# Kernel optimization log

Hardware: AMD Instinct MI355X
Metric: run time of the kernel (lower is better)

The kernel has to match this reference:

```python
import jax, jax.numpy as jnp
import numpy as np

C = 2048
EPS = 1e-12


def conv1x1(x, w, b):
    # x: [B,C_in,H,W], w: [C_out,C_in], b: [C_out]
    return jnp.einsum('oc,bchw->bohw', w, x) + b[None, :, None, None]


def unfold3x3(x):
    # torch F.unfold(kernel=3, padding=1): output [B, C*9, H*W],
    # feature order (c, ki, kj) with c slowest.
    B, Cc, H, W = x.shape
    xp = jnp.pad(x, ((0, 0), (0, 0), (1, 1), (1, 1)))
    patches = jnp.stack([xp[:, :, ki:ki + H, kj:kj + W]
                         for ki in range(3) for kj in range(3)], axis=2)  # [B,C,9,H,W]
    return patches.reshape(B, Cc * 9, H * W)


def fold3x3(u, H, W):
    # torch F.fold(kernel=3, padding=1): overlap-add. u: [B, C*9, H*W]
    B = u.shape[0]
    Cc = u.shape[1] // 9
    t = u.reshape(B, Cc, 3, 3, H, W)
    out = jnp.zeros((B, Cc, H + 2, W + 2), dtype=u.dtype)
    for ki in range(3):
        for kj in range(3):
            out = out.at[:, :, ki:ki + H, kj:kj + W].add(t[:, :, ki, kj])
    return out[:, :, 1:1 + H, 1:1 + W]


def l2norm(x, axis):
    n = jnp.sqrt(jnp.sum(x * x, axis=axis, keepdims=True))
    return x / jnp.maximum(n, EPS)


def setup_inputs() -> dict:
    key = jax.random.key(0)
    ks = jax.random.split(key, 8)
    B, H, W = 4, 24, 24
    s = 0.02
    return {
        'part_ref': jax.random.normal(ks[0], (B, C, H, W), jnp.float32),
        'part_target': jax.random.normal(ks[1], (B, C, H, W), jnp.float32),
        'wq': jax.random.normal(ks[2], (C, C), jnp.float32) * s,
        'bq': jnp.zeros((C,), jnp.float32),
        'wk': jax.random.normal(ks[3], (C, C), jnp.float32) * s,
        'bk': jnp.zeros((C,), jnp.float32),
        'wt': jax.random.normal(ks[4], (C, 2 * C), jnp.float32) * s,
        'bt': jnp.zeros((C,), jnp.float32),
    }


def reference(part_ref, part_target, wq, bq, wk, bk, wt, bt):
    B, _, H, W = part_ref.shape
    part_target_o = part_target
    k = conv1x1(part_ref, wk, bk)
    q = conv1x1(part_target, wq, bq)

    tgt_unf = unfold3x3(q)        # [B, C*9, L]
    ref_unf1 = unfold3x3(k)       # [B, C*9, L]

    ref_n = l2norm(jnp.transpose(ref_unf1, (0, 2, 1)), axis=2)  # [B, L, C*9]
    tgt_n = l2norm(tgt_unf, axis=1)                              # [B, C*9, L]

    R = jnp.einsum('blc,bcm->blm', ref_n, tgt_n)  # [B, L_ref, L_tgt]
    R_star = jnp.max(R, axis=1)                   # [B, L]
    R_arg = jnp.argmax(R, axis=1)                 # [B, L]

    # gather best ref patch per target location along dim 2
    T_unf = jnp.take_along_axis(ref_unf1, R_arg[:, None, :], axis=2)  # [B, C*9, L]
    T_part = fold3x3(T_unf, H, W) / 9.0

    S = R_star.reshape(B, 1, H, W)
    x_res = jnp.concatenate((q, T_part), axis=1)  # [B, 2C, H, W]
    res = conv1x1(x_res, wt, bt) * S + part_target_o
    return res
```

## Files before the change

kernel.cpp:

```cpp
#include <hip/hip_runtime.h>
#include <cstddef>
#include <cstdint>

#define LPIX 576
#define CCH  2048
#define NB   4

typedef __attribute__((ext_vector_type(8))) short short8;
typedef __attribute__((ext_vector_type(4))) float f32x4;
typedef __attribute__((ext_vector_type(4))) unsigned short u16x4;

__device__ __forceinline__ unsigned short f2bf(float f) {
    uint32_t u = __builtin_bit_cast(uint32_t, f);
    u += 0x7fff + ((u >> 16) & 1);
    return (unsigned short)(u >> 16);
}
__device__ __forceinline__ float bf2f(unsigned short s) {
    return __builtin_bit_cast(float, (uint32_t)s << 16);
}

__device__ __forceinline__ void gload_lds16(const void* g, void* l) {
    __builtin_amdgcn_global_load_lds((const __attribute__((address_space(1))) void*)g,
                                     (__attribute__((address_space(3))) void*)l, 16, 0, 0);
}

template<int BM, int BN>
__device__ __forceinline__ void mm_core64(
    const short* __restrict__ Ab, int lda,
    const short* __restrict__ Bb, int ldb,
    int k0, int kend, short* As, short* Bs,
    int m0, int n0, f32x4 (&acc)[BM/32][BN/32])
{
    const int tid  = threadIdx.x;
    const int lane = tid & 63;
    const int w    = tid >> 6;
    const int wm = (w & 1) * (BM / 2);
    const int wn = (w >> 1) * (BN / 2);
    const int l15 = lane & 15;
    const int k8  = (lane >> 4) * 8;
    const int r   = tid >> 2;
    const int kk  = (tid & 3) * 8;

    const short* Aptr[BM / 32]; short* Alds[BM / 32];
    #pragma unroll
    for (int u = 0; u < BM / 32; ++u) {
        const int p = u & 1, g = u >> 1;
        Aptr[u] = Ab + (size_t)(m0 + g * 64 + r) * lda + p * 32 + kk;
        Alds[u] = As + p * BM * 32 + g * 2048 + tid * 8;
    }
    const short* Bptr[BN / 32]; short* Blds[BN / 32];
    #pragma unroll
    for (int u = 0; u < BN / 32; ++u) {
        const int p = u & 1, g = u >> 1;
        Bptr[u] = Bb + (size_t)(n0 + g * 64 + r) * ldb + p * 32 + kk;
        Blds[u] = Bs + p * BN * 32 + g * 2048 + tid * 8;
    }

    for (int c0 = k0; c0 < kend; c0 += 64) {
        #pragma unroll
        for (int u = 0; u < BM / 32; ++u) gload_lds16(Aptr[u] + c0, Alds[u]);
        #pragma unroll
        for (int u = 0; u < BN / 32; ++u) gload_lds16(Bptr[u] + c0, Blds[u]);
        __syncthreads();
        #pragma unroll
        for (int s = 0; s < 2; ++s) {
            short8 fa[BM / 32], fb[BN / 32];
            #pragma unroll
            for (int i = 0; i < BM / 32; ++i)
                fa[i] = *(const short8*)(As + s * BM * 32 + (wm + i * 16 + l15) * 32 + k8);
            #pragma unroll
            for (int j = 0; j < BN / 32; ++j)
                fb[j] = *(const short8*)(Bs + s * BN * 32 + (wn + j * 16 + l15) * 32 + k8);
            #pragma unroll
            for (int i = 0; i < BM / 32; ++i)
                #pragma unroll
                for (int j = 0; j < BN / 32; ++j)
                    acc[i][j] = __builtin_amdgcn_mfma_f32_16x16x32_bf16(fa[i], fb[j], acc[i][j], 0, 0, 0);
        }
        __syncthreads();
    }
}

__global__ __launch_bounds__(256) void wcast2_k(const float* __restrict__ wq,
                                                const float* __restrict__ wk,
                                                short* __restrict__ Wb) {
    const float* W = blockIdx.y ? wk : wq;
    short* D = Wb + (size_t)blockIdx.y * CCH * CCH;
    int i = (blockIdx.x * 256 + threadIdx.x) * 4;
    float4 v = *(const float4*)(W + i);
    u16x4 u;
    u.x = f2bf(v.x); u.y = f2bf(v.y); u.z = f2bf(v.z); u.w = f2bf(v.w);
    *(u16x4*)(D + i) = u;
}

__global__ __launch_bounds__(256) void wcast_k(const float* __restrict__ W,
                                               short* __restrict__ Wb) {
    int i = (blockIdx.x * 256 + threadIdx.x) * 4;
    float4 v = *(const float4*)(W + i);
    u16x4 u;
    u.x = f2bf(v.x); u.y = f2bf(v.y); u.z = f2bf(v.z); u.w = f2bf(v.w);
    *(u16x4*)(Wb + i) = u;
}

__global__ __launch_bounds__(256) void tcast_k(const float* __restrict__ tgt,
                                               const float* __restrict__ ref,
                                               short* __restrict__ T1) {
    __shared__ float tile[32][33];
    const int z = blockIdx.z;
    const int b = z & 3, which = z >> 2;
    const float* X = (which ? ref : tgt) + (size_t)b * CCH * LPIX;
    const int c0 = blockIdx.y * 32;
    const int l0 = blockIdx.x * 32;
    const int tx = threadIdx.x, ty = threadIdx.y;
    #pragma unroll
    for (int j = 0; j < 4; ++j)
        tile[ty + j * 8][tx] = X[(size_t)(c0 + ty + j * 8) * LPIX + l0 + tx];
    __syncthreads();
    short* D = T1 + ((size_t)(which * NB + b) * LPIX) * CCH;
    #pragma unroll
    for (int j = 0; j < 4; ++j)
        D[(size_t)(l0 + ty + j * 8) * CCH + c0 + tx] = (short)f2bf(tile[tx][ty + j * 8]);
}

__global__ __launch_bounds__(256) void conv_k(
    const short* __restrict__ T1, const short* __restrict__ Wb,
    const float* __restrict__ bq, const float* __restrict__ bk,
    short* __restrict__ x2t, short* __restrict__ kt,
    float* __restrict__ nq, float* __restrict__ nk)
{
    __shared__ short As[64 * 64];
    __shared__ short Bs[128 * 64];
    const int id = blockIdx.x;
    const int xcd = id & 7, slot = id >> 3;
    const int sid = xcd * 4 + slot / 36;
    const int r36 = slot % 36;
    const int which = sid >> 4;
    const int m0 = (r36 % 9) * 64;
    const int n0 = (sid & 15) * 128;
    const int b  = r36 / 9;
    const short* Ab = T1 + (size_t)(which * NB + b) * LPIX * CCH;
    const short* Bb = Wb + (size_t)which * CCH * CCH;
    const float* bias = which ? bk : bq;
    short* Yb = which ? (kt + (size_t)b * LPIX * CCH) : (x2t + (size_t)b * LPIX * 4096);
    float* Nb = (which ? nk : nq) + b * LPIX;
    const int ldy = which ? CCH : 4096;
    f32x4 acc[2][4] = {};
    mm_core64<64, 128>(Ab, CCH, Bb, CCH, 0, CCH, As, Bs, m0, n0, acc);
    const int lane = threadIdx.x & 63, w = threadIdx.x >> 6;
    const int wm = (w & 1) * 32, wn = (w >> 1) * 64;
    const int l15 = lane & 15, quad = lane >> 4;
    float pv[2][4] = {};
    #pragma unroll
    for (int i = 0; i < 2; ++i)
        #pragma unroll
        for (int j = 0; j < 4; ++j) {
            const int gn = n0 + wn + j * 16 + l15;
            const float bi = bias[gn];
            #pragma unroll
            for (int r = 0; r < 4; ++r) {
                const int gm = m0 + wm + i * 16 + quad * 4 + r;
                float v = acc[i][j][r] + bi;
                pv[i][r] += v * v;
                Yb[(size_t)gm * ldy + gn] = (short)f2bf(v);
            }
        }
    #pragma unroll
    for (int i = 0; i < 2; ++i)
        #pragma unroll
        for (int r = 0; r < 4; ++r) {
            float s = pv[i][r];
            #pragma unroll
            for (int m = 1; m < 16; m <<= 1) s += __shfl_xor(s, m);
            if (l15 == 0) {
                const int gm = m0 + wm + i * 16 + quad * 4 + r;
                atomicAdd(&Nb[gm], s);
            }
        }
}

__global__ __launch_bounds__(256) void gram_k(
    const short* __restrict__ kt, const short* __restrict__ x2t,
    float* __restrict__ Mpart)
{
    __shared__ short As[64 * 64];
    __shared__ short Bs[64 * 64];
    const int z = blockIdx.z;
    const int b = z >> 1, kc = z & 1;
    const short* Ab = kt + (size_t)b * LPIX * CCH;
    const short* Bb = x2t + (size_t)b * LPIX * 4096;
    const int m0 = blockIdx.y * 64;
    const int n0 = blockIdx.x * 64;
    f32x4 acc[2][2] = {};
    mm_core64<64, 64>(Ab, CCH, Bb, 4096, kc * 1024, kc * 1024 + 1024, As, Bs, m0, n0, acc);
    float* Mb = Mpart + (size_t)(kc * NB + b) * LPIX * LPIX;
    const int lane = threadIdx.x & 63, w = threadIdx.x >> 6;
    const int wm = (w & 1) * 32, wn = (w >> 1) * 32;
    const int l15 = lane & 15, quad = lane >> 4;
    #pragma unroll
    for (int i = 0; i < 2; ++i)
        #pragma unroll
        for (int j = 0; j < 2; ++j) {
            const int gn = n0 + wn + j * 16 + l15;
            #pragma unroll
            for (int r = 0; r < 4; ++r) {
                const int gm = m0 + wm + i * 16 + quad * 4 + r;
                Mb[(size_t)gm * LPIX + gn] = acc[i][j][r];
            }
        }
}

__global__ __launch_bounds__(256) void fin_k(
    const short* __restrict__ wtb, const short* __restrict__ x2t,
    const float* __restrict__ bt, const float* __restrict__ S,
    const float* __restrict__ PT, float* __restrict__ out)
{
    __shared__ short As[128 * 64];
    __shared__ short Bs[64 * 64];
    const int id = blockIdx.x;
    const int xcd = id & 7, slot = id >> 3;
    const int hi = slot >= 36;
    const int r36 = slot - hi * 36;
    const int m0 = (xcd * 2 + hi) * 128;
    const int n0 = (r36 % 9) * 64;
    const int b  = r36 / 9;
    const short* Bb = x2t + (size_t)b * LPIX * 4096;
    f32x4 acc[4][2] = {};
    mm_core64<128, 64>(wtb, 4096, Bb, 4096, 0, 4096, As, Bs, m0, n0, acc);
    const int lane = threadIdx.x & 63, w = threadIdx.x >> 6;
    const int wm = (w & 1) * 64, wn = (w >> 1) * 32;
    const int l15 = lane & 15, quad = lane >> 4;
    #pragma unroll
    for (int i = 0; i < 4; ++i)
        #pragma unroll
        for (int j = 0; j < 2; ++j) {
            const int gn = n0 + wn + j * 16 + l15;
            const float sv = S[b * LPIX + gn];
            #pragma unroll
            for (int r = 0; r < 4; ++r) {
                const int gm = m0 + wm + i * 16 + quad * 4 + r;
                float v = (acc[i][j][r] + bt[gm]) * sv
                        + PT[((size_t)b * CCH + gm) * LPIX + gn];
                out[((size_t)b * CCH + gm) * LPIX + gn] = v;
            }
        }
}

__global__ __launch_bounds__(256) void argmax1_k(
    const float* __restrict__ Mpart, const float* __restrict__ nk,
    float* __restrict__ Pv, int* __restrict__ Pi)
{
    const int b   = blockIdx.z;
    const int lrb = blockIdx.y;
    const int tx = threadIdx.x, ty = threadIdx.y;
    const int tid = ty * 64 + tx;
    __shared__ float invNkS[24];
    if (tid < 24) {
        const int jr = tid;
        float s = 0.f;
        #pragma unroll
        for (int di = -1; di <= 1; ++di) {
            const int ii = lrb + di;
            if ((unsigned)ii > 23u) continue;
            #pragma unroll
            for (int dj = -1; dj <= 1; ++dj) {
                const int jj = jr + dj;
                if ((unsigned)jj > 23u) continue;
                s += nk[b * LPIX + ii * 24 + jj];
            }
        }
        invNkS[jr] = 1.0f / fmaxf(sqrtf(s), 1e-12f);
    }
    __syncthreads();
    const int lt = blockIdx.x * 64 + tx;
    const int it = lt / 24, jt = lt % 24;
    const float* Mb0 = Mpart + (size_t)b * LPIX * LPIX;
    const float* Mb1 = Mpart + (size_t)(NB + b) * LPIX * LPIX;
    float best = -1e30f; int bidx = 0;
    #pragma unroll
    for (int i = 0; i < 6; ++i) {
        const int jr = ty + i * 4;
        const int lr = lrb * 24 + jr;
        const int base = lr * LPIX + lt;
        float g = 0.f;
        #pragma unroll
        for (int di = -1; di <= 1; ++di) {
            if ((unsigned)(lrb + di) > 23u || (unsigned)(it + di) > 23u) continue;
            #pragma unroll
            for (int dj = -1; dj <= 1; ++dj) {
                if ((unsigned)(jr + dj) > 23u || (unsigned)(jt + dj) > 23u) continue;
                const int o = base + (di * 24 + dj) * (LPIX + 1);
                g += Mb0[o] + Mb1[o];
            }
        }
        float v = g * invNkS[jr];
        if (v > best) { best = v; bidx = lr; }
    }
    __shared__ float rv[4][64];
    __shared__ int   ri[4][64];
    rv[ty][tx] = best; ri[ty][tx] = bidx;
    __syncthreads();
    if (ty == 0) {
        #pragma unroll
        for (int y = 1; y < 4; ++y) {
            float v = rv[y][tx]; int id = ri[y][tx];
            if (v > best || (v == best && id < bidx)) { best = v; bidx = id; }
        }
        Pv[((size_t)b * 24 + lrb) * LPIX + lt] = best;
        Pi[((size_t)b * 24 + lrb) * LPIX + lt] = bidx;
    }
}

__global__ __launch_bounds__(256) void argmax2_k(
    const float* __restrict__ Pv, const int* __restrict__ Pi,
    const float* __restrict__ nq,
    float* __restrict__ S, int* __restrict__ Arg)
{
    int idx = blockIdx.x * 256 + threadIdx.x;
    if (idx >= NB * LPIX) return;
    int b = idx / LPIX, lt = idx % LPIX;
    int it = lt / 24, jt = lt % 24;
    float s = 0.f;
    #pragma unroll
    for (int di = -1; di <= 1; ++di) {
        const int ii = it + di;
        if ((unsigned)ii > 23u) continue;
        #pragma unroll
        for (int dj = -1; dj <= 1; ++dj) {
            const int jj = jt + dj;
            if ((unsigned)jj > 23u) continue;
            s += nq[b * LPIX + ii * 24 + jj];
        }
    }
    const float invNq = 1.0f / fmaxf(sqrtf(s), 1e-12f);
    float best = -1e30f; int bidx = 0;
    #pragma unroll
    for (int c = 0; c < 24; ++c) {
        float v = Pv[((size_t)b * 24 + c) * LPIX + lt];
        int  id = Pi[((size_t)b * 24 + c) * LPIX + lt];
        if (v > best || (v == best && id < bidx)) { best = v; bidx = id; }
    }
    S[idx]   = best * invNq;
    Arg[idx] = bidx;
}

__global__ __launch_bounds__(256) void gather_k(
    const short* __restrict__ kt, const int* __restrict__ Arg,
    short* __restrict__ x2t)
{
    const int id = blockIdx.x;
    const int xcd = id & 7, slot = id >> 3;
    const int b  = xcd >> 1;
    const int l0 = ((xcd & 1) * 72 + slot) * 4;
    const int lane = threadIdx.x, ty = threadIdx.y;
    const int tid = ty * 64 + lane;
    __shared__ int tap[4][9];
    if (tid < 36) {
        int px = tid / 9, t9 = tid % 9;
        int l = l0 + px;
        int i = l / 24, j = l % 24;
        int ki = t9 / 3, kj = t9 % 3;
        int ip = i + 1 - ki, jp = j + 1 - kj;
        int off = -1;
        if (ip >= 0 && ip < 24 && jp >= 0 && jp < 24) {
            int a = Arg[b * LPIX + ip * 24 + jp];
            int rr = a / 24 + ki - 1;
            int cc = a % 24 + kj - 1;
            if (rr >= 0 && rr < 24 && cc >= 0 && cc < 24) off = rr * 24 + cc;
        }
        tap[px][t9] = off;
    }
    __syncthreads();
    const int l = l0 + ty;
    const short* Kb = kt + (size_t)b * LPIX * CCH;
    short* dst = x2t + ((size_t)b * LPIX + l) * 4096 + CCH;
    int t[9];
    #pragma unroll
    for (int i = 0; i < 9; ++i) t[i] = tap[ty][i];
    const float inv9 = 1.0f / 9.0f;
    #pragma unroll
    for (int j = 0; j < 8; ++j) {
        int c = (lane + j * 64) * 4;
        float s0 = 0.f, s1 = 0.f, s2 = 0.f, s3 = 0.f;
        #pragma unroll
        for (int t9 = 0; t9 < 9; ++t9) {
            int off = t[t9];
            if (off < 0) continue;
            u16x4 u = *(const u16x4*)(Kb + (size_t)off * CCH + c);
            s0 += bf2f(u.x); s1 += bf2f(u.y); s2 += bf2f(u.z); s3 += bf2f(u.w);
        }
        u16x4 o;
        o.x = f2bf(s0 * inv9); o.y = f2bf(s1 * inv9);
        o.z = f2bf(s2 * inv9); o.w = f2bf(s3 * inv9);
        *(u16x4*)(dst + c) = o;
    }
}

extern "C" void kernel_launch(void* const* d_in, const int* in_sizes, int n_in,
                              void* d_out, int out_size, void* d_ws, size_t ws_size,
                              hipStream_t stream) {
    const float* part_ref = (const float*)d_in[0];
    const float* part_tgt = (const float*)d_in[1];
    const float* wq = (const float*)d_in[2];
    const float* bq = (const float*)d_in[3];
    const float* wk = (const float*)d_in[4];
    const float* bk = (const float*)d_in[5];
    const float* wt = (const float*)d_in[6];
    const float* bt = (const float*)d_in[7];
    float* out = (float*)d_out;

    short* wqb2 = (short*)d_ws;
    short* wtb  = wqb2;
    short* T1   = wqb2 + (size_t)2 * CCH * CCH;
    short* kt   = T1 + (size_t)2 * NB * LPIX * CCH;
    short* x2t  = kt + (size_t)NB * LPIX * CCH;
    float* Mpart = (float*)T1;
    float* nk    = (float*)(x2t + (size_t)NB * LPIX * 4096);
    float* nq    = nk + NB * LPIX;
    float* Sbuf  = nq + NB * LPIX;
    int*   Arg   = (int*)(Sbuf + NB * LPIX);
    float* Pv    = (float*)(Arg + NB * LPIX);
    int*   Pi    = (int*)(Pv + (size_t)24 * NB * LPIX);

    hipMemsetAsync(nk, 0, 2 * NB * LPIX * sizeof(float), stream);

    wcast2_k<<<dim3(4096, 2), 256, 0, stream>>>(wq, wk, wqb2);
    tcast_k<<<dim3(18, 64, 8), dim3(32, 8), 0, stream>>>(part_tgt, part_ref, T1);

    conv_k<<<1152, 256, 0, stream>>>(T1, wqb2, bq, bk, x2t, kt, nq, nk);

    gram_k<<<dim3(9, 9, 8), 256, 0, stream>>>(kt, x2t, Mpart);

    argmax1_k<<<dim3(9, 24, NB), dim3(64, 4), 0, stream>>>(Mpart, nk, Pv, Pi);
    argmax2_k<<<9, 256, 0, stream>>>(Pv, Pi, nq, Sbuf, Arg);

    gather_k<<<576, dim3(64, 4), 0, stream>>>(kt, Arg, x2t);

    wcast_k<<<8192, 256, 0, stream>>>(wt, wtb);
    fin_k<<<576, 256, 0, stream>>>(wtb, x2t, bt, Sbuf, part_tgt, out);
}
```

Measured before the change: 351.6 us.

## Merge batch into row dimension, use 128x128 tiles, split-K final conv with atomics

The conv kernel now treats all four batches as one 2304-row matrix and uses 128x128 tiles, halving the block count and raising reuse per loaded tile. The final 1x1 conv also uses 128x128 tiles over the merged pixel dimension, with K split in two and results accumulated into the output via float atomicAdd. A new init kernel first writes the bias*S + residual term to the output. This trades fewer, larger GEMM blocks for atomic traffic on the output, an extra full pass over it, and nondeterministic summation order.

```diff
diff --git a/kernel.cpp b/kernel.cpp
--- a/kernel.cpp
+++ b/kernel.cpp
@@ -5,6 +5,7 @@
 #define LPIX 576
 #define CCH  2048
 #define NB   4
+#define LROWS 2304
 
 typedef __attribute__((ext_vector_type(8))) short short8;
 typedef __attribute__((ext_vector_type(4))) float f32x4;
@@ -128,30 +129,27 @@
     short* __restrict__ x2t, short* __restrict__ kt,
     float* __restrict__ nq, float* __restrict__ nk)
 {
-    __shared__ short As[64 * 64];
+    __shared__ short As[128 * 64];
     __shared__ short Bs[128 * 64];
     const int id = blockIdx.x;
     const int xcd = id & 7, slot = id >> 3;
-    const int sid = xcd * 4 + slot / 36;
-    const int r36 = slot % 36;
+    const int sid = xcd * 4 + slot / 18;
+    const int r18 = slot % 18;
     const int which = sid >> 4;
-    const int m0 = (r36 % 9) * 64;
     const int n0 = (sid & 15) * 128;
-    const int b  = r36 / 9;
-    const short* Ab = T1 + (size_t)(which * NB + b) * LPIX * CCH;
+    const int m0 = r18 * 128;
+    const short* Ab = T1 + (size_t)which * LROWS * CCH;
     const short* Bb = Wb + (size_t)which * CCH * CCH;
     const float* bias = which ? bk : bq;
-    short* Yb = which ? (kt + (size_t)b * LPIX * CCH) : (x2t + (size_t)b * LPIX * 4096);
-    float* Nb = (which ? nk : nq) + b * LPIX;
-    const int ldy = which ? CCH : 4096;
-    f32x4 acc[2][4] = {};
-    mm_core64<64, 128>(Ab, CCH, Bb, CCH, 0, CCH, As, Bs, m0, n0, acc);
+    float* Nb = which ? nk : nq;
+    f32x4 acc[4][4] = {};
+    mm_core64<128, 128>(Ab, CCH, Bb, CCH, 0, CCH, As, Bs, m0, n0, acc);
     const int lane = threadIdx.x & 63, w = threadIdx.x >> 6;
-    const int wm = (w & 1) * 32, wn = (w >> 1) * 64;
+    const int wm = (w & 1) * 64, wn = (w >> 1) * 64;
     const int l15 = lane & 15, quad = lane >> 4;
-    float pv[2][4] = {};
-    #pragma unroll
-    for (int i = 0; i < 2; ++i)
+    float pv[4][4] = {};
+    #pragma unroll
+    for (int i = 0; i < 4; ++i)
         #pragma unroll
         for (int j = 0; j < 4; ++j) {
             const int gn = n0 + wn + j * 16 + l15;
@@ -161,11 +159,12 @@
                 const int gm = m0 + wm + i * 16 + quad * 4 + r;
                 float v = acc[i][j][r] + bi;
                 pv[i][r] += v * v;
-                Yb[(size_t)gm * ldy + gn] = (short)f2bf(v);
-            }
-        }
-    #pragma unroll
-    for (int i = 0; i < 2; ++i)
+                if (which) kt[(size_t)gm * CCH + gn] = (short)f2bf(v);
+                else       x2t[(size_t)gm * 4096 + gn] = (short)f2bf(v);
+            }
+        }
+    #pragma unroll
+    for (int i = 0; i < 4; ++i)
         #pragma unroll
         for (int r = 0; r < 4; ++r) {
             float s = pv[i][r];
@@ -209,38 +208,52 @@
         }
 }
 
+__global__ __launch_bounds__(256) void initout_k(
+    const float* __restrict__ bt, const float* __restrict__ S,
+    const float* __restrict__ PT, float* __restrict__ out)
+{
+    const int idx = blockIdx.x * 256 + threadIdx.x;
+    const int l4 = idx % 144;
+    const int o  = (idx / 144) % CCH;
+    const int b  = idx / (144 * CCH);
+    const float bi = bt[o];
+    float4 sv = *(const float4*)(S + b * LPIX + l4 * 4);
+    float4 pv = *(const float4*)(PT + ((size_t)b * CCH + o) * LPIX + l4 * 4);
+    float4 ov;
+    ov.x = bi * sv.x + pv.x; ov.y = bi * sv.y + pv.y;
+    ov.z = bi * sv.z + pv.z; ov.w = bi * sv.w + pv.w;
+    *(float4*)(out + ((size_t)b * CCH + o) * LPIX + l4 * 4) = ov;
+}
+
 __global__ __launch_bounds__(256) void fin_k(
     const short* __restrict__ wtb, const short* __restrict__ x2t,
-    const float* __restrict__ bt, const float* __restrict__ S,
-    const float* __restrict__ PT, float* __restrict__ out)
+    const float* __restrict__ S, float* __restrict__ out)
 {
     __shared__ short As[128 * 64];
-    __shared__ short Bs[64 * 64];
+    __shared__ short Bs[128 * 64];
     const int id = blockIdx.x;
     const int xcd = id & 7, slot = id >> 3;
-    const int hi = slot >= 36;
-    const int r36 = slot - hi * 36;
-    const int m0 = (xcd * 2 + hi) * 128;
-    const int n0 = (r36 % 9) * 64;
-    const int b  = r36 / 9;
-    const short* Bb = x2t + (size_t)b * LPIX * 4096;
-    f32x4 acc[4][2] = {};
-    mm_core64<128, 64>(wtb, 4096, Bb, 4096, 0, 4096, As, Bs, m0, n0, acc);
+    const int sid = xcd * 2 + slot / 36;
+    const int rem = slot % 36;
+    const int kc = rem / 18;
+    const int m0 = sid * 128;
+    const int n0 = (rem % 18) * 128;
+    f32x4 acc[4][4] = {};
+    mm_core64<128, 128>(wtb, 4096, x2t, 4096, kc * 2048, kc * 2048 + 2048, As, Bs, m0, n0, acc);
     const int lane = threadIdx.x & 63, w = threadIdx.x >> 6;
-    const int wm = (w & 1) * 64, wn = (w >> 1) * 32;
+    const int wm = (w & 1) * 64, wn = (w >> 1) * 64;
     const int l15 = lane & 15, quad = lane >> 4;
     #pragma unroll
     for (int i = 0; i < 4; ++i)
         #pragma unroll
-        for (int j = 0; j < 2; ++j) {
+        for (int j = 0; j < 4; ++j) {
             const int gn = n0 + wn + j * 16 + l15;
-            const float sv = S[b * LPIX + gn];
+            const int b = gn / LPIX, l = gn - b * LPIX;
+            const float sv = S[gn];
             #pragma unroll
             for (int r = 0; r < 4; ++r) {
                 const int gm = m0 + wm + i * 16 + quad * 4 + r;
-                float v = (acc[i][j][r] + bt[gm]) * sv
-                        + PT[((size_t)b * CCH + gm) * LPIX + gn];
-                out[((size_t)b * CCH + gm) * LPIX + gn] = v;
+                atomicAdd(&out[((size_t)b * CCH + gm) * LPIX + l], acc[i][j][r] * sv);
             }
         }
 }
@@ -411,30 +424,32 @@
     short* wqb2 = (short*)d_ws;
     short* wtb  = wqb2;
     short* T1   = wqb2 + (size_t)2 * CCH * CCH;
-    short* kt   = T1 + (size_t)2 * NB * LPIX * CCH;
-    short* x2t  = kt + (size_t)NB * LPIX * CCH;
+    short* kt   = T1 + (size_t)2 * LROWS * CCH;
+    short* x2t  = kt + (size_t)LROWS * CCH;
     float* Mpart = (float*)T1;
-    float* nk    = (float*)(x2t + (size_t)NB * LPIX * 4096);
-    float* nq    = nk + NB * LPIX;
-    float* Sbuf  = nq + NB * LPIX;
-    int*   Arg   = (int*)(Sbuf + NB * LPIX);
-    float* Pv    = (float*)(Arg + NB * LPIX);
-    int*   Pi    = (int*)(Pv + (size_t)24 * NB * LPIX);
-
-    hipMemsetAsync(nk, 0, 2 * NB * LPIX * sizeof(float), stream);
+    float* nk    = (float*)(x2t + (size_t)LROWS * 4096);
+    float* nq    = nk + LROWS;
+    float* Sbuf  = nq + LROWS;
+    int*   Arg   = (int*)(Sbuf + LROWS);
+    float* Pv    = (float*)(Arg + LROWS);
+    int*   Pi    = (int*)(Pv + (size_t)24 * LROWS);
+
+    hipMemsetAsync(nk, 0, 2 * LROWS * sizeof(float), stream);
 
     wcast2_k<<<dim3(4096, 2), 256, 0, stream>>>(wq, wk, wqb2);
     tcast_k<<<dim3(18, 64, 8), dim3(32, 8), 0, stream>>>(part_tgt, part_ref, T1);
 
-    conv_k<<<1152, 256, 0, stream>>>(T1, wqb2, bq, bk, x2t, kt, nq, nk);
+    conv_k<<<576, 256, 0, stream>>>(T1, wqb2, bq, bk, x2t, kt, nq, nk);
 
     gram_k<<<dim3(9, 9, 8), 256, 0, stream>>>(kt, x2t, Mpart);
 
     argmax1_k<<<dim3(9, 24, NB), dim3(64, 4), 0, stream>>>(Mpart, nk, Pv, Pi);
     argmax2_k<<<9, 256, 0, stream>>>(Pv, Pi, nq, Sbuf, Arg);
 
+    initout_k<<<4608, 256, 0, stream>>>(bt, Sbuf, part_tgt, out);
+
     gather_k<<<576, dim3(64, 4), 0, stream>>>(kt, Arg, x2t);
 
     wcast_k<<<8192, 256, 0, stream>>>(wt, wtb);
-    fin_k<<<576, 256, 0, stream>>>(wtb, x2t, bt, Sbuf, part_tgt, out);
-}
+    fin_k<<<576, 256, 0, stream>>>(wtb, x2t, Sbuf, out);
+}
```

New measurement: 415.5 us. 18.2% more time.
